# Kernel tuning notes

Hardware: AMD Instinct MI355X
Metric: run time of the kernel (lower is better)

Reference implementation:

```python
import jax, jax.numpy as jnp
import numpy as np

BN_EPS = 1e-5
N_NODES = 100000
N_EDGES = 1600000
D = 128


def setup_inputs() -> dict:
    key = jax.random.key(0)
    ks = jax.random.split(key, 8)
    h = jax.random.normal(ks[0], (N_NODES, D), dtype=jnp.float32)
    snorm_n = jax.random.uniform(ks[1], (N_NODES, 1), dtype=jnp.float32)
    eps = jnp.zeros((1,), dtype=jnp.float32)
    W1 = jax.random.normal(ks[2], (D, D), dtype=jnp.float32) * (1.0 / np.sqrt(D))
    b1 = jnp.zeros((D,), dtype=jnp.float32)
    W2 = jax.random.normal(ks[3], (D, D), dtype=jnp.float32) * (1.0 / np.sqrt(D))
    b2 = jnp.zeros((D,), dtype=jnp.float32)
    bn_gamma = jnp.ones((D,), dtype=jnp.float32)
    bn_beta = jnp.zeros((D,), dtype=jnp.float32)
    src = jax.random.randint(ks[4], (N_EDGES,), 0, N_NODES, dtype=jnp.int32)
    dst = jax.random.randint(ks[5], (N_EDGES,), 0, N_NODES, dtype=jnp.int32)
    return {"h": h, "snorm_n": snorm_n, "eps": eps, "W1": W1, "b1": b1,
            "W2": W2, "b2": b2, "bn_gamma": bn_gamma, "bn_beta": bn_beta,
            "src": src, "dst": dst}


def reference(h, snorm_n, eps, W1, b1, W2, b2, bn_gamma, bn_beta, src, dst):
    h_in = h
    # message passing: copy_u + sum reduce -> scatter-add of h[src] into dst
    neigh = jax.ops.segment_sum(h[src], dst, num_segments=N_NODES)  # [N, D]
    x = (1.0 + eps[0]) * h + neigh
    # apply_func: 2-layer MLP (Linear -> ReLU -> Linear)
    x = jax.nn.relu(x @ W1 + b1) @ W2 + b2
    # graph norm w.r.t. graph sizes
    x = x * snorm_n
    # batch norm (training-mode batch statistics over nodes)
    mean = jnp.mean(x, axis=0)
    var = jnp.var(x, axis=0)
    x = (x - mean) * jax.lax.rsqrt(var + BN_EPS) * bn_gamma + bn_beta
    x = jax.nn.relu(x)
    # residual (in_dim == out_dim)
    x = h_in + x
    # dropout p=0.0 -> identity
    return x
```

## Files before the change

### kernel.cpp

```cpp
#include <hip/hip_runtime.h>

#define D 128
#define NN 100000
#define NE 1600000
#define SCAN_NBLK 98
#define GT_ROWS 128
#define GEMM_NT ((NN + GT_ROWS - 1) / GT_ROWS)
#define GEMM_GRID 512
#define NRANGE 8
#define RANGE_SZ 12500
#define STREAM_CAP 204800
#define BINA_GRID 256
#define FILLB_GRID 1024

__global__ void init8_kernel(unsigned int* __restrict__ gcur8)
{
    if (threadIdx.x < NRANGE) gcur8[threadIdx.x] = threadIdx.x * STREAM_CAP;
}

__global__ __launch_bounds__(256) void bin_count_kernel(
    const int* __restrict__ src, const int* __restrict__ dst,
    int* __restrict__ cnt, unsigned int* __restrict__ gcur8,
    unsigned int* __restrict__ stream)
{
    __shared__ unsigned int cnt8[NRANGE], base8[NRANGE], off8[NRANGE];
    const int tid = threadIdx.x;
    if (tid < NRANGE) cnt8[tid] = 0;
    __syncthreads();
    const int NT4 = NE / 4;
    for (int i4 = blockIdx.x * 256 + tid; i4 < NT4; i4 += BINA_GRID * 256) {
        int4 d = ((const int4*)dst)[i4];
        atomicAdd(&cnt[d.x], 1);
        atomicAdd(&cnt[d.y], 1);
        atomicAdd(&cnt[d.z], 1);
        atomicAdd(&cnt[d.w], 1);
        atomicAdd(&cnt8[d.x / RANGE_SZ], 1u);
        atomicAdd(&cnt8[d.y / RANGE_SZ], 1u);
        atomicAdd(&cnt8[d.z / RANGE_SZ], 1u);
        atomicAdd(&cnt8[d.w / RANGE_SZ], 1u);
    }
    __syncthreads();
    if (tid < NRANGE) {
        base8[tid] = atomicAdd(&gcur8[tid], cnt8[tid]);
        off8[tid]  = 0;
    }
    __syncthreads();
    for (int i4 = blockIdx.x * 256 + tid; i4 < NT4; i4 += BINA_GRID * 256) {
        int4 d = ((const int4*)dst)[i4];
        int4 s = ((const int4*)src)[i4];
        {
            int r = d.x / RANGE_SZ; unsigned dl = (unsigned)(d.x - r * RANGE_SZ);
            unsigned pos = base8[r] + atomicAdd(&off8[r], 1u);
            stream[pos] = (dl << 17) | (unsigned)s.x;
        }
        {
            int r = d.y / RANGE_SZ; unsigned dl = (unsigned)(d.y - r * RANGE_SZ);
            unsigned pos = base8[r] + atomicAdd(&off8[r], 1u);
            stream[pos] = (dl << 17) | (unsigned)s.y;
        }
        {
            int r = d.z / RANGE_SZ; unsigned dl = (unsigned)(d.z - r * RANGE_SZ);
            unsigned pos = base8[r] + atomicAdd(&off8[r], 1u);
            stream[pos] = (dl << 17) | (unsigned)s.z;
        }
        {
            int r = d.w / RANGE_SZ; unsigned dl = (unsigned)(d.w - r * RANGE_SZ);
            unsigned pos = base8[r] + atomicAdd(&off8[r], 1u);
            stream[pos] = (dl << 17) | (unsigned)s.w;
        }
    }
}

__global__ __launch_bounds__(256) void scan_local_kernel(
    const int* __restrict__ cnt, int* __restrict__ pre, int* __restrict__ blkSum)
{
    __shared__ int lds[256];
    const int t = threadIdx.x;
    const int base = blockIdx.x * 1024 + t * 4;
    int4 v = {0, 0, 0, 0};
    if (base + 3 < NN) v = *(const int4*)&cnt[base];
    else {
        if (base + 0 < NN) v.x = cnt[base + 0];
        if (base + 1 < NN) v.y = cnt[base + 1];
        if (base + 2 < NN) v.z = cnt[base + 2];
        if (base + 3 < NN) v.w = cnt[base + 3];
    }
    const int s = v.x + v.y + v.z + v.w;
    lds[t] = s;
    __syncthreads();
    for (int off = 1; off < 256; off <<= 1) {
        int val = 0;
        if (t >= off) val = lds[t - off];
        __syncthreads();
        if (t >= off) lds[t] += val;
        __syncthreads();
    }
    const int excl = lds[t] - s;
    if (t == 255) blkSum[blockIdx.x] = lds[255];
    int4 o;
    o.x = excl;
    o.y = excl + v.x;
    o.z = excl + v.x + v.y;
    o.w = excl + v.x + v.y + v.z;
    if (base + 3 < NN) *(int4*)&pre[base] = o;
    else {
        if (base + 0 < NN) pre[base + 0] = o.x;
        if (base + 1 < NN) pre[base + 1] = o.y;
        if (base + 2 < NN) pre[base + 2] = o.z;
        if (base + 3 < NN) pre[base + 3] = o.w;
    }
}

__global__ __launch_bounds__(128) void scan_blk_kernel(
    const int* __restrict__ blkSum, int* __restrict__ blkOfs)
{
    __shared__ int lds[128];
    const int t = threadIdx.x;
    int s = (t < SCAN_NBLK) ? blkSum[t] : 0;
    lds[t] = s;
    __syncthreads();
    for (int off = 1; off < 128; off <<= 1) {
        int val = 0;
        if (t >= off) val = lds[t - off];
        __syncthreads();
        if (t >= off) lds[t] += val;
        __syncthreads();
    }
    blkOfs[t] = lds[t] - s;
}

__global__ __launch_bounds__(256) void scan_finish_kernel(
    const int* __restrict__ pre, const int* __restrict__ blkOfs,
    int* __restrict__ row_start, int* __restrict__ cursor)
{
    int n = blockIdx.x * 256 + threadIdx.x;
    if (n > NN) return;
    int v = (n == NN) ? NE : pre[n] + blkOfs[n >> 10];
    row_start[n] = v;
    if (n < NN) cursor[n] = v;
}

__global__ __launch_bounds__(256) void fill_kernel(
    const unsigned int* __restrict__ stream, const unsigned int* __restrict__ gcur8,
    int* __restrict__ cursor, int* __restrict__ eidx)
{
    const int r = blockIdx.x & 7;
    const int chunk = blockIdx.x >> 3;
    const unsigned s1 = gcur8[r];
    const unsigned stride = (FILLB_GRID / 8) * 256;
    for (unsigned i = (unsigned)r * STREAM_CAP + chunk * 256 + threadIdx.x;
         i < s1; i += stride) {
        unsigned p = stream[i];
        int s  = (int)(p & 0x1FFFFu);
        int dn = r * RANGE_SZ + (int)(p >> 17);
        int pos = atomicAdd(&cursor[dn], 1);
        eidx[pos] = s;
    }
}

__global__ __launch_bounds__(256) void gather_kernel(
    const float* __restrict__ h, const int* __restrict__ row_start,
    const int* __restrict__ eidx, const float* __restrict__ epsp,
    float* __restrict__ x)
{
    int gid  = blockIdx.x * 256 + threadIdx.x;
    int node = gid >> 5;
    int lane = gid & 31;
    if (node >= NN) return;
    const int s0 = row_start[node];
    const int s1 = row_start[node + 1];
    const float sc = 1.0f + epsp[0];
    float4 hv = ((const float4*)(h + (size_t)node * D))[lane];
    float ax = sc * hv.x, ay = sc * hv.y, az = sc * hv.z, aw = sc * hv.w;
    float bx = 0.f, by = 0.f, bz = 0.f, bw = 0.f;
    int e = s0;
    for (; e + 1 < s1; e += 2) {
        int sa = eidx[e];
        int sb = eidx[e + 1];
        float4 va = ((const float4*)(h + (size_t)sa * D))[lane];
        float4 vb = ((const float4*)(h + (size_t)sb * D))[lane];
        ax += va.x; ay += va.y; az += va.z; aw += va.w;
        bx += vb.x; by += vb.y; bz += vb.z; bw += vb.w;
    }
    if (e < s1) {
        int sa = eidx[e];
        float4 va = ((const float4*)(h + (size_t)sa * D))[lane];
        ax += va.x; ay += va.y; az += va.z; aw += va.w;
    }
    float4 o = {ax + bx, ay + by, az + bz, aw + bw};
    ((float4*)(x + (size_t)node * D))[lane] = o;
}

template <int MODE>
__global__ __launch_bounds__(256, 2) void gemm_kernel(
    const float* __restrict__ xin, const float* __restrict__ W,
    const float* __restrict__ bias, const float* __restrict__ snorm,
    float* __restrict__ out, double* __restrict__ stats)
{
    __shared__ float xb[D * GT_ROWS];
    const int tid = threadIdx.x;
    const int cg = tid & 15;
    const int rg = tid >> 4;
    const int ca = cg * 4;
    const int cb = 64 + cg * 4;
    const float4* Wv = (const float4*)W;

    float4 bva = ((const float4*)bias)[cg];
    float4 bvb = ((const float4*)bias)[16 + cg];

    float ssum[8], ssq[8];
#pragma unroll
    for (int j = 0; j < 8; ++j) { ssum[j] = 0.f; ssq[j] = 0.f; }

    float4 rstg[16];
    auto LOADT = [&](int t) {
        const int row0 = t * GT_ROWS;
#pragma unroll
        for (int i = 0; i < 16; ++i) {
            int idx = tid + i * 256;
            int row = idx >> 5;
            int kc  = idx & 31;
            int grow = row0 + row;
            rstg[i] = (grow < NN)
                ? ((const float4*)(xin + (size_t)grow * D))[kc]
                : make_float4(0.f, 0.f, 0.f, 0.f);
        }
    };
    auto WRITET = [&]() {
#pragma unroll
        for (int i = 0; i < 16; ++i) {
            int idx = tid + i * 256;
            int row = idx >> 5;
            int kc  = idx & 31;
            int c4  = (row >> 2) ^ (kc & 7);
            float v[4] = {rstg[i].x, rstg[i].y, rstg[i].z, rstg[i].w};
#pragma unroll
            for (int j = 0; j < 4; ++j)
                xb[(kc * 4 + j) * GT_ROWS + c4 * 4 + (row & 3)] = v[j];
        }
    };

    bool first = true;
    for (int t = blockIdx.x; t < GEMM_NT; t += GEMM_GRID) {
        if (first) { LOADT(t); first = false; }
        __syncthreads();
        WRITET();
        __syncthreads();

        float acc[8][8];
#pragma unroll
        for (int i = 0; i < 8; ++i)
#pragma unroll
            for (int j = 0; j < 8; ++j) acc[i][j] = 0.f;

#pragma unroll 4
        for (int k = 0; k < D; ++k) {
            const int sk = (k >> 2) & 7;
            float4 xa = *(const float4*)&xb[k * GT_ROWS + (((rg * 2) ^ sk) << 2)];
            float4 xc = *(const float4*)&xb[k * GT_ROWS + (((rg * 2 + 1) ^ sk) << 2)];
            float4 wa = Wv[k * 32 + cg];
            float4 wb = Wv[k * 32 + 16 + cg];
            float xr[8] = {xa.x, xa.y, xa.z, xa.w, xc.x, xc.y, xc.z, xc.w};
            float wr[8] = {wa.x, wa.y, wa.z, wa.w, wb.x, wb.y, wb.z, wb.w};
#pragma unroll
            for (int i = 0; i < 8; ++i)
#pragma unroll
                for (int j = 0; j < 8; ++j)
                    acc[i][j] = fmaf(xr[i], wr[j], acc[i][j]);
        }

        int tn = t + GEMM_GRID;
        if (tn < GEMM_NT) LOADT(tn);

#pragma unroll
        for (int i = 0; i < 8; ++i) {
            int row = t * GT_ROWS + rg * 8 + i;
            if (row < NN) {
                float oa[4], ob[4];
                if (MODE == 1) {
                    oa[0] = fmaxf(acc[i][0] + bva.x, 0.f);
                    oa[1] = fmaxf(acc[i][1] + bva.y, 0.f);
                    oa[2] = fmaxf(acc[i][2] + bva.z, 0.f);
                    oa[3] = fmaxf(acc[i][3] + bva.w, 0.f);
                    ob[0] = fmaxf(acc[i][4] + bvb.x, 0.f);
                    ob[1] = fmaxf(acc[i][5] + bvb.y, 0.f);
                    ob[2] = fmaxf(acc[i][6] + bvb.z, 0.f);
                    ob[3] = fmaxf(acc[i][7] + bvb.w, 0.f);
                } else {
                    const float sn = snorm[row];
                    oa[0] = (acc[i][0] + bva.x) * sn;
                    oa[1] = (acc[i][1] + bva.y) * sn;
                    oa[2] = (acc[i][2] + bva.z) * sn;
                    oa[3] = (acc[i][3] + bva.w) * sn;
                    ob[0] = (acc[i][4] + bvb.x) * sn;
                    ob[1] = (acc[i][5] + bvb.y) * sn;
                    ob[2] = (acc[i][6] + bvb.z) * sn;
                    ob[3] = (acc[i][7] + bvb.w) * sn;
#pragma unroll
                    for (int j = 0; j < 4; ++j) {
                        ssum[j]     += oa[j];  ssq[j]     += oa[j] * oa[j];
                        ssum[4 + j] += ob[j];  ssq[4 + j] += ob[j] * ob[j];
                    }
                }
                float* op = out + (size_t)row * D;
                *(float4*)&op[ca] = *(float4*)&oa[0];
                *(float4*)&op[cb] = *(float4*)&ob[0];
            }
        }
    }

    if (MODE == 2) {
        float* red = xb;
        __syncthreads();
#pragma unroll
        for (int j = 0; j < 4; ++j) {
            red[rg * D + ca + j] = ssum[j];
            red[rg * D + cb + j] = ssum[4 + j];
        }
        __syncthreads();
        if (tid < D) {
            float s = 0.f;
#pragma unroll
            for (int r = 0; r < 16; ++r) s += red[r * D + tid];
            atomicAdd(&stats[tid], (double)s);
        }
        __syncthreads();
#pragma unroll
        for (int j = 0; j < 4; ++j) {
            red[rg * D + ca + j] = ssq[j];
            red[rg * D + cb + j] = ssq[4 + j];
        }
        __syncthreads();
        if (tid < D) {
            float s = 0.f;
#pragma unroll
            for (int r = 0; r < 16; ++r) s += red[r * D + tid];
            atomicAdd(&stats[D + tid], (double)s);
        }
    }
}

__global__ void bn_prep_kernel(const double* __restrict__ stats,
                               const float* __restrict__ gamma,
                               const float* __restrict__ beta,
                               float* __restrict__ sc_sh)
{
    int c = threadIdx.x;
    double mean = stats[c] * (1.0 / NN);
    double var  = stats[D + c] * (1.0 / NN) - mean * mean;
    float rs = rsqrtf((float)var + 1e-5f);
    float sc = gamma[c] * rs;
    sc_sh[c]     = sc;
    sc_sh[D + c] = beta[c] - (float)mean * sc;
}

__global__ __launch_bounds__(256) void finalize_kernel(
    const float* __restrict__ y, const float* __restrict__ h,
    const float* __restrict__ sc_sh, float* __restrict__ out)
{
    int i  = blockIdx.x * 256 + threadIdx.x;
    int cf = i & 31;
    float4 yv = ((const float4*)y)[i];
    float4 hv = ((const float4*)h)[i];
    float4 sc = ((const float4*)sc_sh)[cf];
    float4 sh = ((const float4*)(sc_sh + D))[cf];
    float4 o;
    o.x = hv.x + fmaxf(fmaf(yv.x, sc.x, sh.x), 0.0f);
    o.y = hv.y + fmaxf(fmaf(yv.y, sc.y, sh.y), 0.0f);
    o.z = hv.z + fmaxf(fmaf(yv.z, sc.z, sh.z), 0.0f);
    o.w = hv.w + fmaxf(fmaf(yv.w, sc.w, sh.w), 0.0f);
    ((float4*)out)[i] = o;
}

extern "C" void kernel_launch(void* const* d_in, const int* in_sizes, int n_in,
                              void* d_out, int out_size, void* d_ws, size_t ws_size,
                              hipStream_t stream)
{
    const float* h     = (const float*)d_in[0];
    const float* snorm = (const float*)d_in[1];
    const float* eps   = (const float*)d_in[2];
    const float* W1    = (const float*)d_in[3];
    const float* b1    = (const float*)d_in[4];
    const float* W2    = (const float*)d_in[5];
    const float* b2    = (const float*)d_in[6];
    const float* gamma = (const float*)d_in[7];
    const float* beta  = (const float*)d_in[8];
    const int*   src   = (const int*)d_in[9];
    const int*   dst   = (const int*)d_in[10];
    float* out = (float*)d_out;

    char* ws = (char*)d_ws;
    const size_t BUF_BYTES = (size_t)NN * D * sizeof(float);
    float*  buf       = (float*)ws;
    double* stats     = (double*)(ws + BUF_BYTES);
    float*  sc_sh     = (float*)(ws + BUF_BYTES + 2048);
    char*   p         = ws + BUF_BYTES + 4096;
    int*    cnt       = (int*)p;            p += (size_t)NN * 4;
    int*    pre       = (int*)p;            p += (size_t)NN * 4;
    int*    row_start = (int*)p;            p += (size_t)(NN + 4) * 4;
    int*    cursor    = (int*)p;            p += (size_t)NN * 4;
    int*    blkSum    = (int*)p;            p += 512;
    int*    blkOfs    = (int*)p;            p += 512;
    unsigned int* gcur8  = (unsigned int*)p;  p += 256;
    int*    eidx      = (int*)p;            p += (size_t)NE * 4;
    unsigned int* stream8 = (unsigned int*)p;

    hipMemsetAsync(cnt, 0, (size_t)NN * 4, stream);
    hipMemsetAsync(stats, 0, 2048, stream);
    init8_kernel<<<1, 64, 0, stream>>>(gcur8);

    bin_count_kernel<<<BINA_GRID, 256, 0, stream>>>(src, dst, cnt, gcur8, stream8);
    scan_local_kernel<<<SCAN_NBLK, 256, 0, stream>>>(cnt, pre, blkSum);
    scan_blk_kernel<<<1, 128, 0, stream>>>(blkSum, blkOfs);
    scan_finish_kernel<<<(NN + 256) / 256 + 1, 256, 0, stream>>>(pre, blkOfs, row_start, cursor);
    fill_kernel<<<FILLB_GRID, 256, 0, stream>>>(stream8, gcur8, cursor, eidx);

    gather_kernel<<<NN * 32 / 256, 256, 0, stream>>>(h, row_start, eidx, eps, buf);

    gemm_kernel<1><<<GEMM_GRID, 256, 0, stream>>>(buf, W1, b1, nullptr, buf, nullptr);
    gemm_kernel<2><<<GEMM_GRID, 256, 0, stream>>>(buf, W2, b2, snorm, buf, stats);

    bn_prep_kernel<<<1, D, 0, stream>>>(stats, gamma, beta, sc_sh);
    finalize_kernel<<<NN * D / 4 / 256, 256, 0, stream>>>(buf, h, sc_sh, out);
}
```

Before: 577.9 us.

## Stage weights in LDS with K-split GEMM and privatize degree counters

The GEMM now splits K into two halves of 64. It stages both the activation slice and the matching weight slice in shared memory, with a double-buffered register prefetch, instead of reading W from global memory inside the inner loop. Separately, degree counting uses 8 private count arrays, chosen by block index and aliased onto the eidx buffer, and the scan sums them. This reduces global atomic contention on cnt. In exchange it adds an extra barrier pair per tile, a larger memset, and 8x reads in the scan.

```diff
diff --git a/kernel.cpp b/kernel.cpp
--- a/kernel.cpp
+++ b/kernel.cpp
@@ -20,20 +20,21 @@
 
 __global__ __launch_bounds__(256) void bin_count_kernel(
     const int* __restrict__ src, const int* __restrict__ dst,
-    int* __restrict__ cnt, unsigned int* __restrict__ gcur8,
+    int* __restrict__ cnt8x, unsigned int* __restrict__ gcur8,
     unsigned int* __restrict__ stream)
 {
     __shared__ unsigned int cnt8[NRANGE], base8[NRANGE], off8[NRANGE];
     const int tid = threadIdx.x;
     if (tid < NRANGE) cnt8[tid] = 0;
     __syncthreads();
+    int* mycnt = cnt8x + (size_t)(blockIdx.x & 7) * NN;
     const int NT4 = NE / 4;
     for (int i4 = blockIdx.x * 256 + tid; i4 < NT4; i4 += BINA_GRID * 256) {
         int4 d = ((const int4*)dst)[i4];
-        atomicAdd(&cnt[d.x], 1);
-        atomicAdd(&cnt[d.y], 1);
-        atomicAdd(&cnt[d.z], 1);
-        atomicAdd(&cnt[d.w], 1);
+        atomicAdd(&mycnt[d.x], 1);
+        atomicAdd(&mycnt[d.y], 1);
+        atomicAdd(&mycnt[d.z], 1);
+        atomicAdd(&mycnt[d.w], 1);
         atomicAdd(&cnt8[d.x / RANGE_SZ], 1u);
         atomicAdd(&cnt8[d.y / RANGE_SZ], 1u);
         atomicAdd(&cnt8[d.z / RANGE_SZ], 1u);
@@ -72,18 +73,26 @@
 }
 
 __global__ __launch_bounds__(256) void scan_local_kernel(
-    const int* __restrict__ cnt, int* __restrict__ pre, int* __restrict__ blkSum)
+    const int* __restrict__ cnt8x, int* __restrict__ pre, int* __restrict__ blkSum)
 {
     __shared__ int lds[256];
     const int t = threadIdx.x;
     const int base = blockIdx.x * 1024 + t * 4;
     int4 v = {0, 0, 0, 0};
-    if (base + 3 < NN) v = *(const int4*)&cnt[base];
-    else {
-        if (base + 0 < NN) v.x = cnt[base + 0];
-        if (base + 1 < NN) v.y = cnt[base + 1];
-        if (base + 2 < NN) v.z = cnt[base + 2];
-        if (base + 3 < NN) v.w = cnt[base + 3];
+    if (base + 3 < NN) {
+#pragma unroll
+        for (int r = 0; r < NRANGE; ++r) {
+            int4 c = *(const int4*)&cnt8x[(size_t)r * NN + base];
+            v.x += c.x; v.y += c.y; v.z += c.z; v.w += c.w;
+        }
+    } else {
+#pragma unroll
+        for (int r = 0; r < NRANGE; ++r) {
+            if (base + 0 < NN) v.x += cnt8x[(size_t)r * NN + base + 0];
+            if (base + 1 < NN) v.y += cnt8x[(size_t)r * NN + base + 1];
+            if (base + 2 < NN) v.z += cnt8x[(size_t)r * NN + base + 2];
+            if (base + 3 < NN) v.w += cnt8x[(size_t)r * NN + base + 3];
+        }
     }
     const int s = v.x + v.y + v.z + v.w;
     lds[t] = s;
@@ -197,13 +206,13 @@
     const float* __restrict__ bias, const float* __restrict__ snorm,
     float* __restrict__ out, double* __restrict__ stats)
 {
-    __shared__ float xb[D * GT_ROWS];
+    __shared__ float wl[64 * D];
+    __shared__ float xb[64 * D];
     const int tid = threadIdx.x;
     const int cg = tid & 15;
     const int rg = tid >> 4;
     const int ca = cg * 4;
     const int cb = 64 + cg * 4;
-    const float4* Wv = (const float4*)W;
 
     float4 bva = ((const float4*)bias)[cg];
     float4 bvb = ((const float4*)bias)[16 + cg];
@@ -212,65 +221,81 @@
 #pragma unroll
     for (int j = 0; j < 8; ++j) { ssum[j] = 0.f; ssq[j] = 0.f; }
 
-    float4 rstg[16];
-    auto LOADT = [&](int t) {
+    float4 xs[8], wsg[8];
+    auto LOADG = [&](int t, int hh) {
         const int row0 = t * GT_ROWS;
 #pragma unroll
-        for (int i = 0; i < 16; ++i) {
+        for (int i = 0; i < 8; ++i) {
             int idx = tid + i * 256;
-            int row = idx >> 5;
-            int kc  = idx & 31;
+            int row = idx >> 4;
+            int kc  = idx & 15;
             int grow = row0 + row;
-            rstg[i] = (grow < NN)
-                ? ((const float4*)(xin + (size_t)grow * D))[kc]
+            xs[i] = (grow < NN)
+                ? ((const float4*)(xin + (size_t)grow * D))[hh * 16 + kc]
                 : make_float4(0.f, 0.f, 0.f, 0.f);
         }
+#pragma unroll
+        for (int i = 0; i < 8; ++i) {
+            int idx = tid + i * 256;
+            int k  = idx >> 5;
+            int c4 = idx & 31;
+            wsg[i] = ((const float4*)(W + (size_t)(hh * 64 + k) * D))[c4];
+        }
     };
-    auto WRITET = [&]() {
-#pragma unroll
-        for (int i = 0; i < 16; ++i) {
+    auto WRITEL = [&]() {
+#pragma unroll
+        for (int i = 0; i < 8; ++i) {
             int idx = tid + i * 256;
-            int row = idx >> 5;
-            int kc  = idx & 31;
-            int c4  = (row >> 2) ^ (kc & 7);
-            float v[4] = {rstg[i].x, rstg[i].y, rstg[i].z, rstg[i].w};
+            int row = idx >> 4;
+            int kc  = idx & 15;
+            float v[4] = {xs[i].x, xs[i].y, xs[i].z, xs[i].w};
 #pragma unroll
             for (int j = 0; j < 4; ++j)
-                xb[(kc * 4 + j) * GT_ROWS + c4 * 4 + (row & 3)] = v[j];
+                xb[(kc * 4 + j) * D + (row ^ (kc << 2))] = v[j];
+        }
+#pragma unroll
+        for (int i = 0; i < 8; ++i) {
+            int idx = tid + i * 256;
+            int k  = idx >> 5;
+            int c4 = idx & 31;
+            *(float4*)&wl[k * D + c4 * 4] = wsg[i];
         }
     };
 
     bool first = true;
     for (int t = blockIdx.x; t < GEMM_NT; t += GEMM_GRID) {
-        if (first) { LOADT(t); first = false; }
-        __syncthreads();
-        WRITET();
-        __syncthreads();
-
         float acc[8][8];
 #pragma unroll
         for (int i = 0; i < 8; ++i)
 #pragma unroll
             for (int j = 0; j < 8; ++j) acc[i][j] = 0.f;
 
-#pragma unroll 4
-        for (int k = 0; k < D; ++k) {
-            const int sk = (k >> 2) & 7;
-            float4 xa = *(const float4*)&xb[k * GT_ROWS + (((rg * 2) ^ sk) << 2)];
-            float4 xc = *(const float4*)&xb[k * GT_ROWS + (((rg * 2 + 1) ^ sk) << 2)];
-            float4 wa = Wv[k * 32 + cg];
-            float4 wb = Wv[k * 32 + 16 + cg];
-            float xr[8] = {xa.x, xa.y, xa.z, xa.w, xc.x, xc.y, xc.z, xc.w};
-            float wr[8] = {wa.x, wa.y, wa.z, wa.w, wb.x, wb.y, wb.z, wb.w};
-#pragma unroll
-            for (int i = 0; i < 8; ++i)
-#pragma unroll
-                for (int j = 0; j < 8; ++j)
-                    acc[i][j] = fmaf(xr[i], wr[j], acc[i][j]);
-        }
-
-        int tn = t + GEMM_GRID;
-        if (tn < GEMM_NT) LOADT(tn);
+#pragma unroll 1
+        for (int hh = 0; hh < 2; ++hh) {
+            if (first) { LOADG(t, 0); first = false; }
+            __syncthreads();
+            WRITEL();
+            int nt = (hh == 0) ? t : t + GEMM_GRID;
+            int nh = hh ^ 1;
+            if (nt < GEMM_NT) LOADG(nt, nh);
+            __syncthreads();
+
+#pragma unroll 8
+            for (int k = 0; k < 64; ++k) {
+                const int V = ((k >> 2) & 15) << 2;
+                float4 xa = *(const float4*)&xb[k * D + ((rg * 8) ^ V)];
+                float4 xc = *(const float4*)&xb[k * D + ((rg * 8 + 4) ^ V)];
+                float4 wa = *(const float4*)&wl[k * D + ca];
+                float4 wb = *(const float4*)&wl[k * D + cb];
+                float xr[8] = {xa.x, xa.y, xa.z, xa.w, xc.x, xc.y, xc.z, xc.w};
+                float wr[8] = {wa.x, wa.y, wa.z, wa.w, wb.x, wb.y, wb.z, wb.w};
+#pragma unroll
+                for (int i = 0; i < 8; ++i)
+#pragma unroll
+                    for (int j = 0; j < 8; ++j)
+                        acc[i][j] = fmaf(xr[i], wr[j], acc[i][j]);
+            }
+        }
 
 #pragma unroll
         for (int i = 0; i < 8; ++i) {
@@ -395,7 +420,6 @@
     double* stats     = (double*)(ws + BUF_BYTES);
     float*  sc_sh     = (float*)(ws + BUF_BYTES + 2048);
     char*   p         = ws + BUF_BYTES + 4096;
-    int*    cnt       = (int*)p;            p += (size_t)NN * 4;
     int*    pre       = (int*)p;            p += (size_t)NN * 4;
     int*    row_start = (int*)p;            p += (size_t)(NN + 4) * 4;
     int*    cursor    = (int*)p;            p += (size_t)NN * 4;
@@ -404,13 +428,14 @@
     unsigned int* gcur8  = (unsigned int*)p;  p += 256;
     int*    eidx      = (int*)p;            p += (size_t)NE * 4;
     unsigned int* stream8 = (unsigned int*)p;
-
-    hipMemsetAsync(cnt, 0, (size_t)NN * 4, stream);
+    int*    cnt8x     = eidx;
+
+    hipMemsetAsync(cnt8x, 0, (size_t)NRANGE * NN * 4, stream);
     hipMemsetAsync(stats, 0, 2048, stream);
     init8_kernel<<<1, 64, 0, stream>>>(gcur8);
 
-    bin_count_kernel<<<BINA_GRID, 256, 0, stream>>>(src, dst, cnt, gcur8, stream8);
-    scan_local_kernel<<<SCAN_NBLK, 256, 0, stream>>>(cnt, pre, blkSum);
+    bin_count_kernel<<<BINA_GRID, 256, 0, stream>>>(src, dst, cnt8x, gcur8, stream8);
+    scan_local_kernel<<<SCAN_NBLK, 256, 0, stream>>>(cnt8x, pre, blkSum);
     scan_blk_kernel<<<1, 128, 0, stream>>>(blkSum, blkOfs);
     scan_finish_kernel<<<(NN + 256) / 256 + 1, 256, 0, stream>>>(pre, blkOfs, row_start, cursor);
     fill_kernel<<<FILLB_GRID, 256, 0, stream>>>(stream8, gcur8, cursor, eidx);
```

Result: faster. 532.4 us (-7.9%).
